# Kernel optimization log

Measured on AMD Instinct MI355X. Metric: run time of the kernel, lower is better.

The kernel has to match this reference:

```python
import jax, jax.numpy as jnp
import numpy as np

B, S, H, L, NH, F, V, K, R = 64, 512, 256, 4, 8, 1024, 50265, 8, 25
DH = H // NH
EPS = 1e-5


def layernorm(x, g, b):
    mu = x.mean(-1, keepdims=True)
    var = ((x - mu) ** 2).mean(-1, keepdims=True)
    return (x - mu) * jax.lax.rsqrt(var + EPS) * g + b


def setup_inputs() -> dict:
    key = jax.random.key(0)
    ks = jax.random.split(key, 24)
    input_ids = jax.random.randint(ks[0], (B, S), 0, V, dtype=jnp.int64)
    # prefix attention mask with variable valid lengths (ragged sequences)
    lengths = jax.random.randint(ks[1], (B,), 16, S + 1)
    attention_mask = (jnp.arange(S)[None, :] < lengths[:, None]).astype(jnp.int32)
    sub_indices = jax.random.randint(ks[2], (B, K), 0, S, dtype=jnp.int64)
    obj_indices = jax.random.randint(ks[3], (B, K), 0, S, dtype=jnp.int64)
    sub_counts = jax.random.randint(ks[4], (B,), 0, K + 1, dtype=jnp.int32)
    obj_counts = jax.random.randint(ks[5], (B,), 0, K + 1, dtype=jnp.int32)
    sc = 0.02
    p = {
        'emb': jax.random.normal(ks[6], (V, H), jnp.float32) * sc,
        'Wqkv': jax.random.normal(ks[7], (L, H, 3 * H), jnp.float32) * sc,
        'bqkv': jnp.zeros((L, 3 * H), jnp.float32),
        'Wo': jax.random.normal(ks[8], (L, H, H), jnp.float32) * sc,
        'bo': jnp.zeros((L, H), jnp.float32),
        'ln1_g': jnp.ones((L, H), jnp.float32), 'ln1_b': jnp.zeros((L, H), jnp.float32),
        'ln2_g': jnp.ones((L, H), jnp.float32), 'ln2_b': jnp.zeros((L, H), jnp.float32),
        'W1': jax.random.normal(ks[9], (L, H, F), jnp.float32) * sc,
        'b1': jnp.zeros((L, F), jnp.float32),
        'W2': jax.random.normal(ks[10], (L, F, H), jnp.float32) * sc,
        'b2': jnp.zeros((L, H), jnp.float32),
        'lnf_g': jnp.ones((H,), jnp.float32), 'lnf_b': jnp.zeros((H,), jnp.float32),
        'mW1': jax.random.normal(ks[11], (3 * H, H), jnp.float32) * sc,
        'mb1': jnp.zeros((H,), jnp.float32),
        'mW2': jax.random.normal(ks[12], (H, R), jnp.float32) * sc,
        'mb2': jnp.zeros((R,), jnp.float32),
    }
    return dict(input_ids=input_ids, attention_mask=attention_mask,
                sub_indices=sub_indices, sub_counts=sub_counts,
                obj_indices=obj_indices, obj_counts=obj_counts, **p)


def _encoder(input_ids, attention_mask, emb, Wqkv, bqkv, Wo, bo,
             ln1_g, ln1_b, ln2_g, ln2_b, W1, b1, W2, b2, lnf_g, lnf_b):
    x = emb[input_ids]  # [B,S,H]
    kbias = jnp.where(attention_mask[:, None, None, :] > 0, 0.0, -1e9)  # mask keys
    scale = 1.0 / np.sqrt(DH)
    for l in range(L):  # small fixed layer loop
        qkv = x @ Wqkv[l] + bqkv[l]
        q, k, v = jnp.split(qkv, 3, axis=-1)
        q = q.reshape(B, S, NH, DH).transpose(0, 2, 1, 3)
        k = k.reshape(B, S, NH, DH).transpose(0, 2, 1, 3)
        v = v.reshape(B, S, NH, DH).transpose(0, 2, 1, 3)
        scores = jnp.einsum('bhqd,bhkd->bhqk', q, k) * scale + kbias
        attn = jax.nn.softmax(scores, axis=-1)
        o = jnp.einsum('bhqk,bhkd->bhqd', attn, v).transpose(0, 2, 1, 3).reshape(B, S, H)
        x = layernorm(x + o @ Wo[l] + bo[l], ln1_g[l], ln1_b[l])
        h = jax.nn.relu(x @ W1[l] + b1[l]) @ W2[l] + b2[l]
        x = layernorm(x + h, ln2_g[l], ln2_b[l])
    return layernorm(x, lnf_g, lnf_b)


def _pooled(seq, idx, counts):
    g = jnp.take_along_axis(seq, idx[:, :, None], axis=1)  # [B,K,H]
    m = (jnp.arange(K)[None, :] < counts[:, None]).astype(seq.dtype)
    s = (g * m[:, :, None]).sum(1)
    c = counts.astype(seq.dtype)[:, None]
    return jnp.where(c > 0, s / jnp.maximum(c, 1.0), 0.0)  # zeros if no indices


def reference(input_ids, attention_mask, sub_indices, sub_counts, obj_indices, obj_counts,
              emb, Wqkv, bqkv, Wo, bo, ln1_g, ln1_b, ln2_g, ln2_b,
              W1, b1, W2, b2, lnf_g, lnf_b, mW1, mb1, mW2, mb2):
    seq = _encoder(input_ids, attention_mask, emb, Wqkv, bqkv, Wo, bo,
                   ln1_g, ln1_b, ln2_g, ln2_b, W1, b1, W2, b2, lnf_g, lnf_b)
    sub = _pooled(seq, sub_indices, sub_counts)
    obj = _pooled(seq, obj_indices, obj_counts)
    mask = attention_mask.astype(seq.dtype)
    lens = mask.sum(1)[:, None]
    story = jnp.where(lens > 0, (seq * mask[:, :, None]).sum(1) / jnp.maximum(lens, 1.0),
                      seq.mean(1))
    feat = jnp.concatenate([sub, obj, story], axis=-1)  # [B,3H]
    logits = jax.nn.relu(feat @ mW1 + mb1) @ mW2 + mb2
    return logits
```

## Files before the change

### kernel.cpp

```cpp
#include <hip/hip_runtime.h>
#include <hip/hip_bf16.h>


typedef __hip_bfloat16 bf16;
typedef __attribute__((ext_vector_type(8))) short short8;
typedef __attribute__((ext_vector_type(4))) float f32x4;

#define S_LEN 512
#define H_DIM 256
#define NTOK  32768
#define QSCALE 0.25503488f

__device__ __forceinline__ void gload_lds16(const void* g, void* l) {
  __builtin_amdgcn_global_load_lds(
      (const __attribute__((address_space(1))) unsigned int*)g,
      (__attribute__((address_space(3))) unsigned int*)l, 16, 0, 0);
}

__device__ __forceinline__ unsigned short f2bu(float x) {
  bf16 t = __float2bfloat16(x);
  return *reinterpret_cast<unsigned short*>(&t);
}

__global__ __launch_bounds__(64) void lens_kernel(
    const int* __restrict__ amask, int* __restrict__ ntiles,
    int* __restrict__ lenb) {
  const int b = blockIdx.x, t = threadIdx.x;
  int c = 0;
#pragma unroll
  for (int i = 0; i < 8; ++i) c += amask[b * S_LEN + t + i * 64];
#pragma unroll
  for (int off = 1; off < 64; off <<= 1) c += __shfl_xor(c, off);
  if (t == 0) {
    lenb[b] = c;
    ntiles[b] = (c + 63) >> 6;
  }
}

__global__ __launch_bounds__(64) void order_kernel(
    const int* __restrict__ ntiles, int* __restrict__ ordb) {
  const int b = threadIdx.x;
  const int ntb = ntiles[b];
  int rank = 0;
  for (int j = 0; j < 64; ++j) {
    const int ntj = __shfl(ntb, j);
    rank += (ntj > ntb) || (ntj == ntb && j < b);
  }
  ordb[rank] = b;
}

__global__ __launch_bounds__(256) void tcast_kernel(
    const float* __restrict__ in, bf16* __restrict__ out, int K, int N) {
  const int l = blockIdx.z;
  in  += (size_t)l * K * N;
  out += (size_t)l * K * N;
  __shared__ float t[32][33];
  const int n0 = blockIdx.x * 32, k0 = blockIdx.y * 32;
  const int c = threadIdx.x & 31, r = threadIdx.x >> 5;
#pragma unroll
  for (int rr = r; rr < 32; rr += 8)
    t[rr][c] = in[(size_t)(k0 + rr) * N + n0 + c];
  __syncthreads();
#pragma unroll
  for (int rr = r; rr < 32; rr += 8)
    out[(size_t)(n0 + rr) * K + k0 + c] = __float2bfloat16(t[c][rr]);
}

__global__ __launch_bounds__(256) void embed_kernel(
    const int* __restrict__ ids, const float* __restrict__ emb,
    float* __restrict__ X, bf16* __restrict__ Xb) {
  size_t i4 = (size_t)blockIdx.x * 256 + threadIdx.x;
  int tok = (int)(i4 >> 6);
  int d4  = (int)(i4 & 63);
  float4 v = *(const float4*)&emb[(size_t)ids[tok] * H_DIM + d4 * 4];
  *(float4*)&X[i4 * 4] = v;
  ushort4 pk;
  pk.x = f2bu(v.x); pk.y = f2bu(v.y); pk.z = f2bu(v.z); pk.w = f2bu(v.w);
  *(ushort4*)&Xb[i4 * 4] = pk;
}

template<int MODE, bool RELU>
__global__ __launch_bounds__(256) void hgemm_kernel(
    const bf16* __restrict__ A, const bf16* __restrict__ Bt,
    const float* __restrict__ bias, float* __restrict__ Cf,
    bf16* __restrict__ Cb, bf16* __restrict__ Vt,
    int M, int N, int K) {
  __shared__ __align__(16) bf16 As[2][4096];
  __shared__ __align__(16) bf16 Bs[2][4096];
  const int tid = threadIdx.x;
  const int wv = tid >> 6, ln = tid & 63;
  const int fr = ln & 15, g4 = ln >> 4;
  const int wr = wv >> 1, wc = wv & 1;
  const int m0 = blockIdx.y * 128, n0 = blockIdx.x * 128;
  const int lr = tid >> 2, lk = (tid & 3) * 8;

#define STAGE_G(buf, kk) do {                                                  \
    const int kof_ = (kk) * 32;                                                \
    gload_lds16(A  + (size_t)(m0 + lr) * K + kof_ + lk,                        \
                &As[(buf)][wv * 512]);                                         \
    gload_lds16(A  + (size_t)(m0 + 64 + lr) * K + kof_ + lk,                   \
                &As[(buf)][2048 + wv * 512]);                                  \
    gload_lds16(Bt + (size_t)(n0 + lr) * K + kof_ + lk,                        \
                &Bs[(buf)][wv * 512]);                                         \
    gload_lds16(Bt + (size_t)(n0 + 64 + lr) * K + kof_ + lk,                   \
                &Bs[(buf)][2048 + wv * 512]);                                  \
  } while (0)

  f32x4 acc[4][4];
#pragma unroll
  for (int i = 0; i < 4; ++i)
#pragma unroll
    for (int j = 0; j < 4; ++j)
      acc[i][j] = (f32x4){0.f, 0.f, 0.f, 0.f};

  const int NT = K >> 5;
  STAGE_G(0, 0);
  __syncthreads();
  int cur = 0;
  for (int kt = 0; kt < NT; ++kt) {
    if (kt + 1 < NT) STAGE_G(cur ^ 1, kt + 1);
    short8 af[4], bfv[4];
#pragma unroll
    for (int i = 0; i < 4; ++i)
      af[i] = *(const short8*)&As[cur][(wr * 64 + i * 16 + fr) * 32 + g4 * 8];
#pragma unroll
    for (int j = 0; j < 4; ++j)
      bfv[j] = *(const short8*)&Bs[cur][(wc * 64 + j * 16 + fr) * 32 + g4 * 8];
#pragma unroll
    for (int i = 0; i < 4; ++i)
#pragma unroll
      for (int j = 0; j < 4; ++j)
        acc[i][j] = __builtin_amdgcn_mfma_f32_16x16x32_bf16(
            af[i], bfv[j], acc[i][j], 0, 0, 0);
    __syncthreads();
    cur ^= 1;
  }
#undef STAGE_G

  const int crow = g4 * 4, ccol = fr;
#pragma unroll
  for (int j = 0; j < 4; ++j) {
    const int n = n0 + wc * 64 + j * 16 + ccol;
    const float bv = bias[n];
#pragma unroll
    for (int i = 0; i < 4; ++i) {
      const int mbase = m0 + wr * 64 + i * 16 + crow;
#pragma unroll
      for (int r = 0; r < 4; ++r) {
        float o = acc[i][j][r] + bv;
        if (RELU) o = fmaxf(o, 0.f);
        const int m = mbase + r;
        if (MODE == 1) {
          Cb[(size_t)m * N + n] = __float2bfloat16(o);
        } else {
          if (n < 512) {
            const float oo = (n < 256) ? o * QSCALE : o;
            Cb[(size_t)m * 768 + n] = __float2bfloat16(oo);
          } else {
            const int hd = n - 512, hh = hd >> 5, dd = hd & 31;
            const int bb = m >> 9, ss = m & 511;
            const int ssw = (ss & ~63) | ((ss & 63) ^ ((dd & 7) << 3));
            Vt[(((size_t)bb * 8 + hh) * 32 + dd) * 512 + ssw] =
                __float2bfloat16(o);
          }
        }
      }
    }
  }
}

__global__ __launch_bounds__(256) void hgemm_ln_kernel(
    const bf16* __restrict__ A, const bf16* __restrict__ Bt,
    const float* __restrict__ bias, float* __restrict__ X,
    bf16* __restrict__ Xb, const float* __restrict__ g,
    const float* __restrict__ bt, int K) {
  __shared__ __align__(16) bf16 As[2][2048];
  __shared__ __align__(16) bf16 Bs[2][8192];
  __shared__ float rsum[4][64];
  __shared__ float rsq[4][64];
  const int tid = threadIdx.x;
  const int wv = tid >> 6;
  const int ln = tid & 63;
  const int fr = ln & 15, g4 = ln >> 4;
  const int m0 = blockIdx.x * 64;

#define STAGE_L(buf, kk) do {                                                  \
    const int kof_ = (kk) * 32;                                                \
    gload_lds16(A + (size_t)(m0 + (tid >> 2)) * K + kof_ + (tid & 3) * 8,      \
                &As[(buf)][wv * 512]);                                         \
    _Pragma("unroll")                                                          \
    for (int e = 0; e < 4; ++e) {                                              \
      const int vt = e * 256 + tid;                                            \
      gload_lds16(Bt + (size_t)(vt >> 2) * K + kof_ + (vt & 3) * 8,            \
                  &Bs[(buf)][e * 2048 + wv * 512]);                            \
    }                                                                          \
  } while (0)

  f32x4 acc[4][4];
#pragma unroll
  for (int i = 0; i < 4; ++i)
#pragma unroll
    for (int j = 0; j < 4; ++j)
      acc[i][j] = (f32x4){0.f, 0.f, 0.f, 0.f};

  const int NT = K >> 5;
  STAGE_L(0, 0);
  __syncthreads();
  int cur = 0;
  for (int kt = 0; kt < NT; ++kt) {
    if (kt + 1 < NT) STAGE_L(cur ^ 1, kt + 1);
    short8 af[4], bfv[4];
#pragma unroll
    for (int i = 0; i < 4; ++i)
      af[i] = *(const short8*)&As[cur][(i * 16 + fr) * 32 + g4 * 8];
#pragma unroll
    for (int j = 0; j < 4; ++j)
      bfv[j] = *(const short8*)&Bs[cur][(wv * 64 + j * 16 + fr) * 32 + g4 * 8];
#pragma unroll
    for (int i = 0; i < 4; ++i)
#pragma unroll
      for (int j = 0; j < 4; ++j)
        acc[i][j] = __builtin_amdgcn_mfma_f32_16x16x32_bf16(
            af[i], bfv[j], acc[i][j], 0, 0, 0);
    __syncthreads();
    cur ^= 1;
  }
#undef STAGE_L

  float gj[4], bj[4], bsj[4];
#pragma unroll
  for (int j = 0; j < 4; ++j) {
    const int n = wv * 64 + j * 16 + fr;
    gj[j] = g[n]; bj[j] = bt[n]; bsj[j] = bias[n];
  }
#pragma unroll
  for (int i = 0; i < 4; ++i) {
#pragma unroll
    for (int r = 0; r < 4; ++r) {
      const int m = m0 + i * 16 + g4 * 4 + r;
#pragma unroll
      for (int j = 0; j < 4; ++j)
        acc[i][j][r] += bsj[j] + X[(size_t)m * 256 + wv * 64 + j * 16 + fr];
    }
  }
#pragma unroll
  for (int i = 0; i < 4; ++i) {
#pragma unroll
    for (int r = 0; r < 4; ++r) {
      float sp = acc[i][0][r] + acc[i][1][r] + acc[i][2][r] + acc[i][3][r];
      float qp = acc[i][0][r] * acc[i][0][r] + acc[i][1][r] * acc[i][1][r] +
                 acc[i][2][r] * acc[i][2][r] + acc[i][3][r] * acc[i][3][r];
#pragma unroll
      for (int off = 1; off < 16; off <<= 1) {
        sp += __shfl_xor(sp, off);
        qp += __shfl_xor(qp, off);
      }
      if (fr == 0) {
        const int ri = i * 16 + g4 * 4 + r;
        rsum[wv][ri] = sp;
        rsq[wv][ri] = qp;
      }
    }
  }
  __syncthreads();
#pragma unroll
  for (int i = 0; i < 4; ++i) {
#pragma unroll
    for (int r = 0; r < 4; ++r) {
      const int ri = i * 16 + g4 * 4 + r;
      const float tot = rsum[0][ri] + rsum[1][ri] + rsum[2][ri] + rsum[3][ri];
      const float tq = rsq[0][ri] + rsq[1][ri] + rsq[2][ri] + rsq[3][ri];
      const float mu = tot * (1.0f / 256.0f);
      const float var = tq * (1.0f / 256.0f) - mu * mu;
      const float rstd = rsqrtf(var + 1e-5f);
      const int m = m0 + ri;
#pragma unroll
      for (int j = 0; j < 4; ++j) {
        const float o = (acc[i][j][r] - mu) * rstd * gj[j] + bj[j];
        const size_t idx = (size_t)m * 256 + wv * 64 + j * 16 + fr;
        X[idx] = o;
        Xb[idx] = __float2bfloat16(o);
      }
    }
  }
}

__global__ __launch_bounds__(256) void attn_mfma_kernel(
    const bf16* __restrict__ QKVb, const bf16* __restrict__ Vt,
    const int* __restrict__ amask, const int* __restrict__ ntiles,
    const int* __restrict__ ordb, bf16* __restrict__ Ob) {
  const int b = ordb[blockIdx.z];
  const int h = blockIdx.y, q0 = blockIdx.x * 64;
  const int tid = threadIdx.x;
  const int wv = tid >> 6, ln = tid & 63;
  const int fr = ln & 15, g4 = ln >> 4;
  const int f8 = (fr & 7) << 3;
  const int bh32 = (b * 8 + h) * 32;
  __shared__ __align__(16) bf16 Ks[2][2048];
  __shared__ __align__(16) bf16 Vs[2][2048];
  __shared__ __align__(16) bf16 Ps[4096];
  __shared__ __align__(16) float Ms[64];

  const int nt = ntiles[b];

#define STAGE_A(buf, kt_) do {                                                 \
    const int k0_ = (kt_) * 64;                                                \
    gload_lds16(QKVb + (size_t)(b * S_LEN + k0_ + (tid >> 2)) * 768 + 256 +    \
                    h * 32 + (tid & 3) * 8,                                    \
                &Ks[(buf)][wv * 512]);                                         \
    gload_lds16(Vt + (size_t)(bh32 + (tid >> 3)) * 512 + k0_ + (tid & 7) * 8,  \
                &Vs[(buf)][wv * 512]);                                         \
    if ((kt_) == nt - 1 && tid < 64)                                           \
      Ms[tid] = (amask[b * S_LEN + k0_ + tid] != 0) ? 0.f : -1e9f;             \
  } while (0)

  gload_lds16(QKVb + (size_t)(b * S_LEN + q0 + (tid >> 2)) * 768 + h * 32 +
                  (tid & 3) * 8,
              &Ps[wv * 512]);
  STAGE_A(0, 0);
  __syncthreads();
  const short8 qb = *(const short8*)&Ps[(wv * 16 + fr) * 32 + g4 * 8];
  __syncthreads();

  f32x4 accO[2];
  accO[0] = (f32x4){0.f, 0.f, 0.f, 0.f};
  accO[1] = (f32x4){0.f, 0.f, 0.f, 0.f};
  float mrun = -1e30f, lrun = 0.f;
  const int srcq = 20 * g4;

  int cur = 0;
  for (int kt = 0; kt < nt; ++kt) {
    if (kt + 1 < nt) STAGE_A(cur ^ 1, kt + 1);
    const bool bnd = (kt == nt - 1);

    f32x4 st[4];
#pragma unroll
    for (int kb = 0; kb < 4; ++kb) {
      const short8 kf = *(const short8*)&Ks[cur][(kb * 16 + fr) * 32 + g4 * 8];
      f32x4 z = (f32x4){0.f, 0.f, 0.f, 0.f};
      st[kb] = __builtin_amdgcn_mfma_f32_16x16x32_bf16(kf, qb, z, 0, 0, 0);
    }

    float p[16];
    if (bnd) {
#pragma unroll
      for (int kb = 0; kb < 4; ++kb) {
        const f32x4 mv = ((const f32x4*)Ms)[kb * 4 + g4];
#pragma unroll
        for (int rr = 0; rr < 4; ++rr) p[kb * 4 + rr] = st[kb][rr] + mv[rr];
      }
    } else {
#pragma unroll
      for (int kb = 0; kb < 4; ++kb)
#pragma unroll
        for (int rr = 0; rr < 4; ++rr) p[kb * 4 + rr] = st[kb][rr];
    }

    const float a0 = fmaxf(fmaxf(p[0], p[1]), p[2]);
    const float a1 = fmaxf(fmaxf(p[3], p[4]), p[5]);
    const float a2 = fmaxf(fmaxf(p[6], p[7]), p[8]);
    const float a3 = fmaxf(fmaxf(p[9], p[10]), p[11]);
    const float a4 = fmaxf(fmaxf(p[12], p[13]), p[14]);
    float mx = fmaxf(fmaxf(fmaxf(a0, a1), fmaxf(a2, a3)), fmaxf(a4, p[15]));
    mx = fmaxf(mx, __shfl_xor(mx, 16));
    mx = fmaxf(mx, __shfl_xor(mx, 32));

    float corr = 1.f;
    if (!__all(mx <= mrun + 8.f)) {
      const float mnew = fmaxf(mrun, mx);
      corr = exp2f(mrun - mnew);
      mrun = mnew;
#pragma unroll
      for (int rr = 0; rr < 4; ++rr) {
        const float cs = __shfl(corr, srcq + rr);
        accO[0][rr] *= cs;
        accO[1][rr] *= cs;
      }
    }

#pragma unroll
    for (int i = 0; i < 16; ++i) p[i] = exp2f(p[i] - mrun);
    const float b0 = p[0] + p[1], b1 = p[2] + p[3], b2 = p[4] + p[5],
                b3 = p[6] + p[7], b4 = p[8] + p[9], b5 = p[10] + p[11],
                b6 = p[12] + p[13], b7 = p[14] + p[15];
    float ps = ((b0 + b1) + (b2 + b3)) + ((b4 + b5) + (b6 + b7));
    ps += __shfl_xor(ps, 16);
    ps += __shfl_xor(ps, 32);
    lrun = lrun * corr + ps;

#pragma unroll
    for (int kb = 0; kb < 4; ++kb) {
      ushort4 w4;
      w4.x = f2bu(p[kb * 4 + 0]);
      w4.y = f2bu(p[kb * 4 + 1]);
      w4.z = f2bu(p[kb * 4 + 2]);
      w4.w = f2bu(p[kb * 4 + 3]);
      *(ushort4*)&Ps[wv * 1024 + fr * 64 + ((kb * 16 + g4 * 4) ^ f8)] = w4;
    }

#pragma unroll
    for (int kk = 0; kk < 2; ++kk) {
      const short8 pa = *(const short8*)
          &Ps[wv * 1024 + fr * 64 + ((kk * 32 + g4 * 8) ^ f8)];
#pragma unroll
      for (int df = 0; df < 2; ++df) {
        const short8 vb = *(const short8*)
            &Vs[cur][(df * 16 + fr) * 64 + ((kk * 32 + g4 * 8) ^ f8)];
        accO[df] = __builtin_amdgcn_mfma_f32_16x16x32_bf16(
            pa, vb, accO[df], 0, 0, 0);
      }
    }
    __syncthreads();
    cur ^= 1;
  }
#undef STAGE_A

  const float inv = 1.0f / lrun;
#pragma unroll
  for (int rr = 0; rr < 4; ++rr) {
    const float iv = __shfl(inv, srcq + rr);
    const int q = q0 + wv * 16 + g4 * 4 + rr;
    const size_t orow = ((size_t)b * S_LEN + q) * H_DIM + h * 32;
    Ob[orow + fr]      = __float2bfloat16(accO[0][rr] * iv);
    Ob[orow + 16 + fr] = __float2bfloat16(accO[1][rr] * iv);
  }
}

__global__ __launch_bounds__(256) void lnf_pool_kernel(
    float* __restrict__ X, const float* __restrict__ g,
    const float* __restrict__ bt, const int* __restrict__ amask,
    float* __restrict__ Pstory) {
  const int b = blockIdx.x, sg = blockIdx.y;
  const int tid = threadIdx.x, wv = tid >> 6, ln = tid & 63;
  const float4 gg = ((const float4*)g)[ln];
  const float4 bb = ((const float4*)bt)[ln];
  float ax = 0.f, ay = 0.f, az = 0.f, aw = 0.f;
  for (int t = wv; t < 64; t += 4) {
    const size_t tok = (size_t)b * S_LEN + sg * 64 + t;
    float4 v = ((const float4*)X)[tok * 64 + ln];
    float s = v.x + v.y + v.z + v.w;
#pragma unroll
    for (int off = 1; off < 64; off <<= 1) s += __shfl_xor(s, off);
    const float mu = s * (1.0f / 256.0f);
    const float dx = v.x - mu, dy = v.y - mu, dz = v.z - mu, dw = v.w - mu;
    float sq = dx * dx + dy * dy + dz * dz + dw * dw;
#pragma unroll
    for (int off = 1; off < 64; off <<= 1) sq += __shfl_xor(sq, off);
    const float rstd = rsqrtf(sq * (1.0f / 256.0f) + 1e-5f);
    float4 o;
    o.x = dx * rstd * gg.x + bb.x;
    o.y = dy * rstd * gg.y + bb.y;
    o.z = dz * rstd * gg.z + bb.z;
    o.w = dw * rstd * gg.w + bb.w;
    ((float4*)X)[tok * 64 + ln] = o;
    if (amask[tok]) { ax += o.x; ay += o.y; az += o.z; aw += o.w; }
  }
  __shared__ float part[4][256];
  part[wv][ln * 4 + 0] = ax;
  part[wv][ln * 4 + 1] = ay;
  part[wv][ln * 4 + 2] = az;
  part[wv][ln * 4 + 3] = aw;
  __syncthreads();
  const float tot = part[0][tid] + part[1][tid] + part[2][tid] + part[3][tid];
  Pstory[((size_t)b * 8 + sg) * 256 + tid] = tot;
}

__global__ __launch_bounds__(256) void poolcls_kernel(
    const float* __restrict__ X, const float* __restrict__ Pstory,
    const int* __restrict__ lenb,
    const int* __restrict__ sub_idx, const int* __restrict__ sub_cnt,
    const int* __restrict__ obj_idx, const int* __restrict__ obj_cnt,
    const float* __restrict__ mW1, const float* __restrict__ mb1,
    const float* __restrict__ mW2, const float* __restrict__ mb2,
    float* __restrict__ out) {
  const int b = blockIdx.x, t = threadIdx.x;
  __shared__ float fs[768];
  __shared__ float hid[256];
  const float* xb = X + (size_t)b * S_LEN * H_DIM;
  {
    float s = 0.f;
#pragma unroll
    for (int i = 0; i < 8; ++i) s += Pstory[((size_t)b * 8 + i) * 256 + t];
    fs[512 + t] = s / (float)lenb[b];
  }
  {
    const int cc = sub_cnt[b];
    float s2 = 0.f;
    for (int j = 0; j < cc; ++j)
      s2 += xb[(size_t)sub_idx[b * 8 + j] * H_DIM + t];
    fs[t] = (cc > 0) ? s2 / (float)cc : 0.f;
  }
  {
    const int cc = obj_cnt[b];
    float s2 = 0.f;
    for (int j = 0; j < cc; ++j)
      s2 += xb[(size_t)obj_idx[b * 8 + j] * H_DIM + t];
    fs[256 + t] = (cc > 0) ? s2 / (float)cc : 0.f;
  }
  __syncthreads();
  float acc = mb1[t];
  for (int k = 0; k < 768; ++k) acc += fs[k] * mW1[(size_t)k * 256 + t];
  hid[t] = fmaxf(acc, 0.f);
  __syncthreads();
  if (t < 25) {
    float o = mb2[t];
    for (int j = 0; j < 256; ++j) o += hid[j] * mW2[j * 25 + t];
    out[b * 25 + t] = o;
  }
}

extern "C" void kernel_launch(void* const* d_in, const int* in_sizes, int n_in,
                              void* d_out, int out_size, void* d_ws, size_t ws_size,
                              hipStream_t stream) {
  const int*   input_ids = (const int*)d_in[0];
  const int*   amask     = (const int*)d_in[1];
  const int*   sub_idx   = (const int*)d_in[2];
  const int*   sub_cnt   = (const int*)d_in[3];
  const int*   obj_idx   = (const int*)d_in[4];
  const int*   obj_cnt   = (const int*)d_in[5];
  const float* emb  = (const float*)d_in[6];
  const float* Wqkv = (const float*)d_in[7];
  const float* bqkv = (const float*)d_in[8];
  const float* Wo   = (const float*)d_in[9];
  const float* bo   = (const float*)d_in[10];
  const float* ln1g = (const float*)d_in[11];
  const float* ln1b = (const float*)d_in[12];
  const float* ln2g = (const float*)d_in[13];
  const float* ln2b = (const float*)d_in[14];
  const float* W1   = (const float*)d_in[15];
  const float* b1   = (const float*)d_in[16];
  const float* W2   = (const float*)d_in[17];
  const float* b2   = (const float*)d_in[18];
  const float* lnfg = (const float*)d_in[19];
  const float* lnfb = (const float*)d_in[20];
  const float* mW1  = (const float*)d_in[21];
  const float* mb1  = (const float*)d_in[22];
  const float* mW2  = (const float*)d_in[23];
  const float* mb2  = (const float*)d_in[24];
  float* out = (float*)d_out;

  char* w = (char*)d_ws;
  float* X    = (float*)w;                         w += (size_t)NTOK * 256 * 4;
  bf16*  Xb   = (bf16*)w;                          w += (size_t)NTOK * 256 * 2;
  bf16*  QKVb = (bf16*)w;                          w += (size_t)NTOK * 768 * 2;
  bf16*  Vtg  = (bf16*)w;                          w += (size_t)NTOK * 256 * 2;
  bf16*  Ob   = (bf16*)w;                          w += (size_t)NTOK * 256 * 2;
  bf16*  Wqkvt= (bf16*)w;                          w += (size_t)4 * 768 * 256 * 2;
  bf16*  Wot  = (bf16*)w;                          w += (size_t)4 * 256 * 256 * 2;
  bf16*  W1t  = (bf16*)w;                          w += (size_t)4 * 1024 * 256 * 2;
  bf16*  W2t  = (bf16*)w;                          w += (size_t)4 * 256 * 1024 * 2;
  float* Pstory = (float*)w;                       w += (size_t)64 * 8 * 256 * 4;
  int*   ntiles = (int*)w;                         w += 256;
  int*   lenb   = (int*)w;                         w += 256;
  int*   ordb   = (int*)w;                         w += 256;
  bf16*  Hb   = QKVb;

  lens_kernel<<<64, 64, 0, stream>>>(amask, ntiles, lenb);
  order_kernel<<<1, 64, 0, stream>>>(ntiles, ordb);
  tcast_kernel<<<dim3(24, 8, 4), 256, 0, stream>>>(Wqkv, Wqkvt, 256, 768);
  tcast_kernel<<<dim3(8, 8, 4), 256, 0, stream>>>(Wo, Wot, 256, 256);
  tcast_kernel<<<dim3(32, 8, 4), 256, 0, stream>>>(W1, W1t, 256, 1024);
  tcast_kernel<<<dim3(8, 32, 4), 256, 0, stream>>>(W2, W2t, 1024, 256);

  embed_kernel<<<8192, 256, 0, stream>>>(input_ids, emb, X, Xb);

  for (int l = 0; l < 4; ++l) {
    const bf16* Wqkvt_l = Wqkvt + (size_t)l * 768 * 256;
    const bf16* Wot_l   = Wot + (size_t)l * 256 * 256;
    const bf16* W1t_l   = W1t + (size_t)l * 1024 * 256;
    const bf16* W2t_l   = W2t + (size_t)l * 256 * 1024;

    hgemm_kernel<2, false><<<dim3(6, 256), 256, 0, stream>>>(
        Xb, Wqkvt_l, bqkv + (size_t)l * 768, nullptr, QKVb, Vtg, NTOK, 768, 256);
    attn_mfma_kernel<<<dim3(8, 8, 64), 256, 0, stream>>>(
        QKVb, Vtg, amask, ntiles, ordb, Ob);
    hgemm_ln_kernel<<<512, 256, 0, stream>>>(
        Ob, Wot_l, bo + (size_t)l * 256, X, Xb,
        ln1g + l * 256, ln1b + l * 256, 256);
    hgemm_kernel<1, true><<<dim3(8, 256), 256, 0, stream>>>(
        Xb, W1t_l, b1 + (size_t)l * 1024, nullptr, Hb, nullptr, NTOK, 1024, 256);
    hgemm_ln_kernel<<<512, 256, 0, stream>>>(
        Hb, W2t_l, b2 + (size_t)l * 256, X, Xb,
        ln2g + l * 256, ln2b + l * 256, 1024);
  }
  lnf_pool_kernel<<<dim3(64, 8), 256, 0, stream>>>(X, lnfg, lnfb, amask, Pstory);
  poolcls_kernel<<<64, 256, 0, stream>>>(X, Pstory, lenb, sub_idx, sub_cnt,
                                         obj_idx, obj_cnt, mW1, mb1, mW2, mb2,
                                         out);
}
```

Baseline: 809.0 us.

## Swizzle LDS tiles for bank-conflict-free MFMA loads and reorder GEMM grid

Applies an XOR swizzle to the 16-byte chunk position when global_load_lds writes A/B/K/Q tiles into LDS, and applies the matching swizzle on the fragment reads. This is meant to remove LDS bank conflicts on the short8 fragment reads in the GEMM, GEMM+LN and attention kernels. Separately, the GEMM grid is transposed so consecutive blocks walk along M and share the same weight column tile, which may improve L2 reuse of the weights. The source addresses change per lane, which slightly alters global coalescing within each 64-byte row segment.

```diff
diff --git a/kernel.cpp b/kernel.cpp
--- a/kernel.cpp
+++ b/kernel.cpp
@@ -78,6 +78,8 @@
   pk.x = f2bu(v.x); pk.y = f2bu(v.y); pk.z = f2bu(v.z); pk.w = f2bu(v.w);
   *(ushort4*)&Xb[i4 * 4] = pk;
 }
+
+#define SRC_CHUNK(tid_) (((tid_) & 3) ^ (((tid_) >> 3) & 3))
 
 template<int MODE, bool RELU>
 __global__ __launch_bounds__(256) void hgemm_kernel(
@@ -91,8 +93,10 @@
   const int wv = tid >> 6, ln = tid & 63;
   const int fr = ln & 15, g4 = ln >> 4;
   const int wr = wv >> 1, wc = wv & 1;
-  const int m0 = blockIdx.y * 128, n0 = blockIdx.x * 128;
-  const int lr = tid >> 2, lk = (tid & 3) * 8;
+  const int m0 = blockIdx.x * 128, n0 = blockIdx.y * 128;
+  const int lr = tid >> 2;
+  const int lk = SRC_CHUNK(tid) * 8;
+  const int rc = (g4 ^ ((fr >> 1) & 3)) * 8;
 
 #define STAGE_G(buf, kk) do {                                                  \
     const int kof_ = (kk) * 32;                                                \
@@ -122,10 +126,10 @@
     short8 af[4], bfv[4];
 #pragma unroll
     for (int i = 0; i < 4; ++i)
-      af[i] = *(const short8*)&As[cur][(wr * 64 + i * 16 + fr) * 32 + g4 * 8];
+      af[i] = *(const short8*)&As[cur][(wr * 64 + i * 16 + fr) * 32 + rc];
 #pragma unroll
     for (int j = 0; j < 4; ++j)
-      bfv[j] = *(const short8*)&Bs[cur][(wc * 64 + j * 16 + fr) * 32 + g4 * 8];
+      bfv[j] = *(const short8*)&Bs[cur][(wc * 64 + j * 16 + fr) * 32 + rc];
 #pragma unroll
     for (int i = 0; i < 4; ++i)
 #pragma unroll
@@ -183,15 +187,17 @@
   const int ln = tid & 63;
   const int fr = ln & 15, g4 = ln >> 4;
   const int m0 = blockIdx.x * 64;
+  const int rc = (g4 ^ ((fr >> 1) & 3)) * 8;
 
 #define STAGE_L(buf, kk) do {                                                  \
     const int kof_ = (kk) * 32;                                                \
-    gload_lds16(A + (size_t)(m0 + (tid >> 2)) * K + kof_ + (tid & 3) * 8,      \
+    gload_lds16(A + (size_t)(m0 + (tid >> 2)) * K + kof_ +                     \
+                    SRC_CHUNK(tid) * 8,                                        \
                 &As[(buf)][wv * 512]);                                         \
     _Pragma("unroll")                                                          \
     for (int e = 0; e < 4; ++e) {                                              \
       const int vt = e * 256 + tid;                                            \
-      gload_lds16(Bt + (size_t)(vt >> 2) * K + kof_ + (vt & 3) * 8,            \
+      gload_lds16(Bt + (size_t)(vt >> 2) * K + kof_ + SRC_CHUNK(vt) * 8,       \
                   &Bs[(buf)][e * 2048 + wv * 512]);                            \
     }                                                                          \
   } while (0)
@@ -212,10 +218,10 @@
     short8 af[4], bfv[4];
 #pragma unroll
     for (int i = 0; i < 4; ++i)
-      af[i] = *(const short8*)&As[cur][(i * 16 + fr) * 32 + g4 * 8];
+      af[i] = *(const short8*)&As[cur][(i * 16 + fr) * 32 + rc];
 #pragma unroll
     for (int j = 0; j < 4; ++j)
-      bfv[j] = *(const short8*)&Bs[cur][(wv * 64 + j * 16 + fr) * 32 + g4 * 8];
+      bfv[j] = *(const short8*)&Bs[cur][(wv * 64 + j * 16 + fr) * 32 + rc];
 #pragma unroll
     for (int i = 0; i < 4; ++i)
 #pragma unroll
@@ -295,6 +301,7 @@
   const int wv = tid >> 6, ln = tid & 63;
   const int fr = ln & 15, g4 = ln >> 4;
   const int f8 = (fr & 7) << 3;
+  const int rc = (g4 ^ ((fr >> 1) & 3)) * 8;
   const int bh32 = (b * 8 + h) * 32;
   __shared__ __align__(16) bf16 Ks[2][2048];
   __shared__ __align__(16) bf16 Vs[2][2048];
@@ -306,7 +313,7 @@
 #define STAGE_A(buf, kt_) do {                                                 \
     const int k0_ = (kt_) * 64;                                                \
     gload_lds16(QKVb + (size_t)(b * S_LEN + k0_ + (tid >> 2)) * 768 + 256 +    \
-                    h * 32 + (tid & 3) * 8,                                    \
+                    h * 32 + SRC_CHUNK(tid) * 8,                               \
                 &Ks[(buf)][wv * 512]);                                         \
     gload_lds16(Vt + (size_t)(bh32 + (tid >> 3)) * 512 + k0_ + (tid & 7) * 8,  \
                 &Vs[(buf)][wv * 512]);                                         \
@@ -315,11 +322,11 @@
   } while (0)
 
   gload_lds16(QKVb + (size_t)(b * S_LEN + q0 + (tid >> 2)) * 768 + h * 32 +
-                  (tid & 3) * 8,
+                  SRC_CHUNK(tid) * 8,
               &Ps[wv * 512]);
   STAGE_A(0, 0);
   __syncthreads();
-  const short8 qb = *(const short8*)&Ps[(wv * 16 + fr) * 32 + g4 * 8];
+  const short8 qb = *(const short8*)&Ps[(wv * 16 + fr) * 32 + rc];
   __syncthreads();
 
   f32x4 accO[2];
@@ -336,7 +343,7 @@
     f32x4 st[4];
 #pragma unroll
     for (int kb = 0; kb < 4; ++kb) {
-      const short8 kf = *(const short8*)&Ks[cur][(kb * 16 + fr) * 32 + g4 * 8];
+      const short8 kf = *(const short8*)&Ks[cur][(kb * 16 + fr) * 32 + rc];
       f32x4 z = (f32x4){0.f, 0.f, 0.f, 0.f};
       st[kb] = __builtin_amdgcn_mfma_f32_16x16x32_bf16(kf, qb, z, 0, 0, 0);
     }
@@ -570,14 +577,14 @@
     const bf16* W1t_l   = W1t + (size_t)l * 1024 * 256;
     const bf16* W2t_l   = W2t + (size_t)l * 256 * 1024;
 
-    hgemm_kernel<2, false><<<dim3(6, 256), 256, 0, stream>>>(
+    hgemm_kernel<2, false><<<dim3(256, 6), 256, 0, stream>>>(
         Xb, Wqkvt_l, bqkv + (size_t)l * 768, nullptr, QKVb, Vtg, NTOK, 768, 256);
     attn_mfma_kernel<<<dim3(8, 8, 64), 256, 0, stream>>>(
         QKVb, Vtg, amask, ntiles, ordb, Ob);
     hgemm_ln_kernel<<<512, 256, 0, stream>>>(
         Ob, Wot_l, bo + (size_t)l * 256, X, Xb,
         ln1g + l * 256, ln1b + l * 256, 256);
-    hgemm_kernel<1, true><<<dim3(8, 256), 256, 0, stream>>>(
+    hgemm_kernel<1, true><<<dim3(256, 8), 256, 0, stream>>>(
         Xb, W1t_l, b1 + (size_t)l * 1024, nullptr, Hb, nullptr, NTOK, 1024, 256);
     hgemm_ln_kernel<<<512, 256, 0, stream>>>(
         Hb, W2t_l, b2 + (size_t)l * 256, X, Xb,
```

Result: faster. 791.1 us (-2.2%).
